# Kernel optimization log

Measured on AMD Instinct MI355X. Metric: run time of the kernel, lower is better.

Reference implementation:

```python
import jax, jax.numpy as jnp
import numpy as np

T = 32400   # bs*H*W BEV queries (1*180*180)
S = 16896   # bs*num_cams*h*w image keys (1*6*32*88)
E = 256     # embed_dim
H = 8       # num_heads
D = 32      # head_dim
MAXL = 32   # max interval length (ref_num_f)


def _mlp(x, w1, b1, w2, b2):
    # nn.Sequential(Linear(E,2E), ReLU, Linear(2E,E))
    return jax.nn.relu(x @ w1 + b1) @ w2 + b2


def setup_inputs() -> dict:
    k0 = jax.random.key(0)
    ks = jax.random.split(k0, 8)
    # ragged interval structure: every BEV cell has an interval of length (idx%32)+1
    lengths = (np.arange(T) % MAXL) + 1
    starts = np.concatenate([np.zeros(1, np.int64), np.cumsum(lengths)[:-1]])
    N = int(lengths.sum())  # 534472 frustum points
    ranks_bev = np.repeat(np.arange(T), lengths)          # sorted by BEV cell
    rng = np.random.default_rng(0)
    ranks_feat = rng.integers(0, S, size=N)               # which key/value row each point reads

    def lin(k, fi, fo):
        return jax.random.normal(k, (fi, fo), jnp.float32) * (1.0 / np.sqrt(fi))

    key_feat = jax.random.normal(ks[1], (S, E), jnp.float32)
    return dict(
        query_depth=jax.random.normal(ks[0], (T, E), jnp.float32),
        key=key_feat,
        value=key_feat,  # module asserts torch.equal(key, value)
        q_w1=lin(ks[2], E, 2 * E), q_b1=jnp.zeros((2 * E,), jnp.float32),
        q_w2=lin(ks[3], 2 * E, E), q_b2=jnp.zeros((E,), jnp.float32),
        k_w1=lin(ks[4], E, 2 * E), k_b1=jnp.zeros((2 * E,), jnp.float32),
        k_w2=lin(ks[5], 2 * E, E), k_b2=jnp.zeros((E,), jnp.float32),
        ranks_feat_f=jnp.asarray(ranks_feat, jnp.int32),
        ranks_bev_f=jnp.asarray(ranks_bev, jnp.int32),
        interval_starts_f=jnp.asarray(starts, jnp.int32),
        interval_lengths_f=jnp.asarray(lengths, jnp.int32),
        ref_num=MAXL,
    )


def reference(query_depth, key, value,
              q_w1, q_b1, q_w2, q_b2,
              k_w1, k_b1, k_w2, k_b2,
              ranks_feat_f, ranks_bev_f,
              interval_starts_f, interval_lengths_f, ref_num):
    scaling = 1.0 / jnp.sqrt(jnp.float32(D))
    q = (_mlp(query_depth, q_w1, q_b1, q_w2, q_b2) * scaling).reshape(T, H, D)
    k = _mlp(key, k_w1, k_b1, k_w2, k_b2).reshape(S, H, D)
    v = value.reshape(S, H, D)

    N = ranks_bev_f.shape[0]
    pt = jnp.arange(N, dtype=jnp.int32)
    # interval id of each point (intervals are contiguous, sorted by start)
    iid = jnp.searchsorted(interval_starts_f, pt, side='right') - 1
    ranks_ref = pt - interval_starts_f[iid]  # within-interval slot, in [0, ref_num)

    # per-point raw attention logit: q[bev] . k[feat] per head  -> [N, H]
    w = jnp.einsum('nhd,nhd->nh', q[ranks_bev_f], k[ranks_feat_f])

    # scatter into ragged weight tensor [T, H, ref_num]; padding masked to -1e9
    attn = jnp.full((T, H, ref_num), -1e9, jnp.float32)
    attn = attn.at[ranks_bev_f, :, ranks_ref].set(w)
    attn = jax.nn.softmax(attn, axis=-1)

    # gather normalized weights back per point and scatter-combine values
    wp = attn[ranks_bev_f, :, ranks_ref]          # [N, H]
    vp = v[ranks_feat_f]                          # [N, H, D]
    out = jnp.zeros((T, H, D), jnp.float32).at[ranks_bev_f].add(wp[:, :, None] * vp)
    return out.reshape(T, E)
```

## Files before the change

### kernel.cpp

```cpp
#include <hip/hip_runtime.h>
#include <hip/hip_bf16.h>
#include <cstdint>
#include <cstddef>

constexpr int T_Q   = 32400;
constexpr int T_PAD = 32512;
constexpr int S_K   = 16896;
constexpr int E_DIM = 256;
constexpr int HID   = 512;

typedef __bf16 bf16x8 __attribute__((ext_vector_type(8)));
typedef float  f32x4  __attribute__((ext_vector_type(4)));
typedef unsigned short ushort8v __attribute__((ext_vector_type(8)));

__device__ __forceinline__ void async16(const __hip_bfloat16* gp, __hip_bfloat16* lp) {
    __builtin_amdgcn_global_load_lds(
        (const __attribute__((address_space(1))) void*)(gp),
        (__attribute__((address_space(3))) void*)(lp), 16, 0, 0);
}

__device__ __forceinline__ float b2f(unsigned short u) {
    return __uint_as_float(((unsigned)u) << 16);
}

constexpr int NB_K = (S_K * E_DIM / 4) / 256;
constexpr int NB_PREP = NB_K + 128;

__global__ __launch_bounds__(256) void prep(
    const float* __restrict__ val_in,
    const float* __restrict__ s0, const float* __restrict__ s1,
    const float* __restrict__ s2, const float* __restrict__ s3,
    __hip_bfloat16* __restrict__ kvB,
    __hip_bfloat16* __restrict__ d0, __hip_bfloat16* __restrict__ d1,
    __hip_bfloat16* __restrict__ d2, __hip_bfloat16* __restrict__ d3) {
    __shared__ float tb[64][65];
    const int b = blockIdx.x;
    const int tid = threadIdx.x;

    if (b < NB_K) {
        int i = (b * 256 + tid) * 4;
        float4 f = *(const float4*)(val_in + i);
        union { ushort4 u4; __hip_bfloat16 bb[4]; } cv;
        cv.bb[0] = __float2bfloat16(f.x);
        cv.bb[1] = __float2bfloat16(f.y);
        cv.bb[2] = __float2bfloat16(f.z);
        cv.bb[3] = __float2bfloat16(f.w);
        int r = i >> 8, c = i & 255;
        *(ushort4*)(kvB + (size_t)r * 512 + 256 + c) = cv.u4;
        return;
    }

    int tloc = b - NB_K;
    int m = tloc >> 5;
    int tt = tloc & 31;
    const float* S = m == 0 ? s0 : m == 1 ? s1 : m == 2 ? s2 : s3;
    __hip_bfloat16* D = m == 0 ? d0 : m == 1 ? d1 : m == 2 ? d2 : d3;
    int Kd, Nd, kt, nt;
    if ((m & 1) == 0) { Kd = 256; Nd = 512; kt = tt & 3; nt = tt >> 2; }
    else              { Kd = 512; Nd = 256; kt = tt & 7; nt = tt >> 3; }
    int tx = tid & 63, ty = tid >> 6;
#pragma unroll
    for (int p = 0; p < 16; ++p) {
        int row = ty * 16 + p;
        tb[row][tx] = S[(size_t)(kt * 64 + row) * Nd + nt * 64 + tx];
    }
    __syncthreads();
#pragma unroll
    for (int p = 0; p < 16; ++p) {
        int row = ty * 16 + p;
        D[(size_t)(nt * 64 + row) * Kd + kt * 64 + tx] = __float2bfloat16(tb[tx][row]);
    }
}


constexpr int MLP_QT = T_PAD / 64;
constexpr int MLP_KT = S_K / 64;
constexpr int MLP_NB = MLP_QT + MLP_KT;

__global__ __launch_bounds__(512) void mlp_fused(
    const float* __restrict__ Aq, const float* __restrict__ Ak,
    const __hip_bfloat16* __restrict__ W1q, const __hip_bfloat16* __restrict__ W1k,
    const __hip_bfloat16* __restrict__ W2q, const __hip_bfloat16* __restrict__ W2k,
    const float* __restrict__ b1q, const float* __restrict__ b1k,
    const float* __restrict__ b2q, const float* __restrict__ b2k,
    __hip_bfloat16* __restrict__ Cq, __hip_bfloat16* __restrict__ Ck,
    float scaleq, int qtiles) {
    __shared__ __align__(16) __hip_bfloat16 As[64 * 256];
    __shared__ __align__(16) __hip_bfloat16 Hs[64 * 256];
    __shared__ __align__(16) __hip_bfloat16 Bsbuf[2][256 * 64];

    const int b = blockIdx.x;
    const bool isq = b < qtiles;
    const float* A  = isq ? Aq : Ak;
    const __hip_bfloat16* W1 = isq ? W1q : W1k;
    const __hip_bfloat16* W2 = isq ? W2q : W2k;
    const float* b1 = isq ? b1q : b1k;
    const float* b2 = isq ? b2q : b2k;
    __hip_bfloat16* C = isq ? Cq : Ck;
    const int ldc = isq ? E_DIM : 512;
    const float scale = isq ? scaleq : 1.0f;
    const int mrow0 = (isq ? b : b - qtiles) * 64;
    const int rowlim = isq ? T_Q : S_K;

    const int tid = threadIdx.x;
    const int w = tid >> 6, l = tid & 63;
    const int lm = l & 15, lq = l >> 4;
    const int wm = w >> 2;
    const int wn4 = w & 3;
    const int srow8 = l >> 3;
    const int u8 = l & 7;
    const int scolB = (u8 ^ srow8) << 3;

    auto issueW1 = [&](int nh, int st, int bi) {
#pragma unroll
        for (int c = 0; c < 4; ++c) {
            int r = w * 32 + c * 8 + srow8;
            async16(W1 + (size_t)(nh * 256 + r) * 256 + st * 64 + scolB,
                    Bsbuf[bi] + (w * 32 + c * 8) * 64);
        }
    };
    auto issueW2 = [&](int nh, int st, int bi) {
#pragma unroll
        for (int c = 0; c < 4; ++c) {
            int r = w * 32 + c * 8 + srow8;
            async16(W2 + (size_t)r * 512 + nh * 256 + st * 64 + scolB,
                    Bsbuf[bi] + (w * 32 + c * 8) * 64);
        }
    };

    issueW1(0, 0, 0);
#pragma unroll
    for (int c = 0; c < 4; ++c) {
        int idx = tid + c * 512;
        int row = idx >> 5;
        int u = idx & 31;
        int gr = mrow0 + row;
        float4 f0 = make_float4(0.f, 0.f, 0.f, 0.f);
        float4 f1 = make_float4(0.f, 0.f, 0.f, 0.f);
        if (gr < rowlim) {
            const float* ap = A + (size_t)gr * 256 + u * 8;
            f0 = *(const float4*)ap;
            f1 = *(const float4*)(ap + 4);
        }
        union { bf16x8 v; __hip_bfloat16 bb[8]; } cv;
        cv.bb[0] = __float2bfloat16(f0.x); cv.bb[1] = __float2bfloat16(f0.y);
        cv.bb[2] = __float2bfloat16(f0.z); cv.bb[3] = __float2bfloat16(f0.w);
        cv.bb[4] = __float2bfloat16(f1.x); cv.bb[5] = __float2bfloat16(f1.y);
        cv.bb[6] = __float2bfloat16(f1.z); cv.bb[7] = __float2bfloat16(f1.w);
        int pu = (u & 24) | ((u & 7) ^ (row & 7));
        *(bf16x8*)(As + row * 256 + pu * 8) = cv.v;
    }
    __syncthreads();

    int cur = 0;
    f32x4 acc2[2][4] = {};

#pragma unroll 1
    for (int nh = 0; nh < 2; ++nh) {
        f32x4 acc[2][4] = {};
#pragma unroll 1
        for (int st = 0; st < 4; ++st) {
            if (st < 3) issueW1(nh, st + 1, cur ^ 1);
            else        issueW2(nh, 0, cur ^ 1);
            const __hip_bfloat16* Bb = Bsbuf[cur];
#pragma unroll
            for (int ks = 0; ks < 2; ++ks) {
                bf16x8 af[2], bfr[4];
#pragma unroll
                for (int mi = 0; mi < 2; ++mi) {
                    int row = wm * 32 + mi * 16 + lm;
                    int un = st * 8 + ks * 4 + lq;
                    int pu = (un & 24) | ((un & 7) ^ (row & 7));
                    af[mi] = *(const bf16x8*)(As + row * 256 + pu * 8);
                }
#pragma unroll
                for (int ni = 0; ni < 4; ++ni) {
                    int brow = wn4 * 64 + ni * 16 + lm;
                    int pu = (ks * 4 + lq) ^ (brow & 7);
                    bfr[ni] = *(const bf16x8*)(Bb + brow * 64 + pu * 8);
                }
#pragma unroll
                for (int mi = 0; mi < 2; ++mi)
#pragma unroll
                    for (int ni = 0; ni < 4; ++ni)
                        acc[mi][ni] = __builtin_amdgcn_mfma_f32_16x16x32_bf16(
                            af[mi], bfr[ni], acc[mi][ni], 0, 0, 0);
            }
            __syncthreads();
            cur ^= 1;
        }

#pragma unroll
        for (int ni = 0; ni < 4; ++ni) {
            int col = wn4 * 64 + ni * 16 + lm;
            float bv = b1[nh * 256 + col];
            int un = col >> 3, el = col & 7;
#pragma unroll
            for (int mi = 0; mi < 2; ++mi) {
#pragma unroll
                for (int r = 0; r < 4; ++r) {
                    int row = wm * 32 + mi * 16 + lq * 4 + r;
                    float vv = fmaxf(acc[mi][ni][r] + bv, 0.f);
                    int pu = (un & 24) | ((un & 7) ^ (row & 7));
                    Hs[row * 256 + pu * 8 + el] = __float2bfloat16(vv);
                }
            }
        }
        __syncthreads();

#pragma unroll 1
        for (int st = 0; st < 4; ++st) {
            if (st < 3)          issueW2(nh, st + 1, cur ^ 1);
            else if (nh == 0)    issueW1(1, 0, cur ^ 1);
            const __hip_bfloat16* Bb = Bsbuf[cur];
#pragma unroll
            for (int ks = 0; ks < 2; ++ks) {
                bf16x8 af[2], bfr[4];
#pragma unroll
                for (int mi = 0; mi < 2; ++mi) {
                    int row = wm * 32 + mi * 16 + lm;
                    int un = st * 8 + ks * 4 + lq;
                    int pu = (un & 24) | ((un & 7) ^ (row & 7));
                    af[mi] = *(const bf16x8*)(Hs + row * 256 + pu * 8);
                }
#pragma unroll
                for (int ni = 0; ni < 4; ++ni) {
                    int brow = wn4 * 64 + ni * 16 + lm;
                    int pu = (ks * 4 + lq) ^ (brow & 7);
                    bfr[ni] = *(const bf16x8*)(Bb + brow * 64 + pu * 8);
                }
#pragma unroll
                for (int mi = 0; mi < 2; ++mi)
#pragma unroll
                    for (int ni = 0; ni < 4; ++ni)
                        acc2[mi][ni] = __builtin_amdgcn_mfma_f32_16x16x32_bf16(
                            af[mi], bfr[ni], acc2[mi][ni], 0, 0, 0);
            }
            __syncthreads();
            cur ^= 1;
        }
    }

#pragma unroll
    for (int ni = 0; ni < 4; ++ni) {
        int col = wn4 * 64 + ni * 16 + lm;
        float bv = b2[col];
#pragma unroll
        for (int mi = 0; mi < 2; ++mi) {
            size_t rowb = (size_t)mrow0 + wm * 32 + mi * 16 + lq * 4;
#pragma unroll
            for (int r = 0; r < 4; ++r) {
                float vv = (acc2[mi][ni][r] + bv) * scale;
                C[(rowb + r) * ldc + col] = __float2bfloat16(vv);
            }
        }
    }
}


#define PREFP(KB, VB, C)                                                     \
    {                                                                        \
        int f_ = __shfl(myf, (C) + half);                                    \
        const __hip_bfloat16* p_ = kv + ((size_t)f_ << 9) + (sub << 3);      \
        KB = *(const ushort8v*)p_;                                           \
        VB = *(const ushort8v*)(p_ + 256);                                   \
    }

#define PROCP(KB, VB, C)                                                     \
    {                                                                        \
        float wv = 0.f;                                                      \
        _Pragma("unroll") for (int i = 0; i < 8; ++i)                        \
            wv = fmaf(qf[i], b2f(KB[i]), wv);                                \
        wv += __shfl_xor(wv, 1);                                             \
        wv += __shfl_xor(wv, 2);                                             \
        float sc = ((C) + half < L) ? wv : -1e30f;                           \
        float so = __shfl_xor(sc, 32);                                       \
        float pm = fmaxf(sc, so);                                            \
        if (__all(pm <= m)) {                                                \
            float p = __expf(sc - m);                                        \
            s += p;                                                          \
            _Pragma("unroll") for (int i = 0; i < 8; ++i)                    \
                a[i] = fmaf(p, b2f(VB[i]), a[i]);                            \
        } else {                                                             \
            float mn = fmaxf(m, pm);                                         \
            float al = __expf(m - mn);                                       \
            float p  = __expf(sc - mn);                                      \
            m = mn;                                                          \
            s = fmaf(s, al, p);                                              \
            _Pragma("unroll") for (int i = 0; i < 8; ++i)                    \
                a[i] = fmaf(p, b2f(VB[i]), a[i] * al);                       \
        }                                                                    \
    }

#define STEPP(KB, VB, J)                                                     \
    if (c + (J) < L) {                                                       \
        PROCP(KB, VB, c + (J));                                              \
        if (c + (J) + 8 < L) PREFP(KB, VB, c + (J) + 8);                     \
    }

constexpr int ATTN_BLOCKS = 2026;

__global__ __launch_bounds__(256) void attn_kernel(
    const __hip_bfloat16* __restrict__ q,
    const __hip_bfloat16* __restrict__ kv,
    const int* __restrict__ rf,
    const int* __restrict__ starts,
    const int* __restrict__ lens,
    float* __restrict__ out) {
    const int wid = threadIdx.x >> 6;
    const int l = threadIdx.x & 63;
    const int sub = l & 31, half = l >> 5;
    const int tstride = gridDim.x * 4;

    for (int t = blockIdx.x * 4 + wid; t < T_Q; t += tstride) {
        int su = __builtin_amdgcn_readfirstlane(starts[t]);
        int L  = __builtin_amdgcn_readfirstlane(lens[t]);

        int li = l < L - 1 ? l : L - 1;
        int myf = rf[su + li];

        ushort8v qu = *(const ushort8v*)(q + (size_t)t * 256 + sub * 8);
        float qf[8];
#pragma unroll
        for (int i = 0; i < 8; ++i) qf[i] = b2f(qu[i]);

        float m = -INFINITY, s = 0.f;
        float a[8] = {0.f, 0.f, 0.f, 0.f, 0.f, 0.f, 0.f, 0.f};

        ushort8v k0 = {}, v0 = {}, k1 = {}, v1 = {};
        ushort8v k2 = {}, v2 = {}, k3 = {}, v3 = {};
        PREFP(k0, v0, 0);
        if (L > 2) PREFP(k1, v1, 2);
        if (L > 4) PREFP(k2, v2, 4);
        if (L > 6) PREFP(k3, v3, 6);

        for (int c = 0; c < L; c += 8) {
            STEPP(k0, v0, 0)
            STEPP(k1, v1, 2)
            STEPP(k2, v2, 4)
            STEPP(k3, v3, 6)
        }

        float st = s + __shfl_xor(s, 32);
#pragma unroll
        for (int i = 0; i < 8; ++i) a[i] += __shfl_xor(a[i], 32);

        if (half) {
            float inv = 1.f / st;
            float* op = out + (size_t)t * 256 + sub * 8;
            float4 o0, o1;
            o0.x = a[0] * inv; o0.y = a[1] * inv; o0.z = a[2] * inv; o0.w = a[3] * inv;
            o1.x = a[4] * inv; o1.y = a[5] * inv; o1.z = a[6] * inv; o1.w = a[7] * inv;
            *(float4*)op = o0;
            *(float4*)(op + 4) = o1;
        }
    }
}

extern "C" void kernel_launch(void* const* d_in, const int* in_sizes, int n_in,
                              void* d_out, int out_size, void* d_ws, size_t ws_size,
                              hipStream_t stream) {
    const float* q_in   = (const float*)d_in[0];
    const float* key_in = (const float*)d_in[1];
    const float* val_in = (const float*)d_in[2];
    const float* q_w1   = (const float*)d_in[3];
    const float* q_b1   = (const float*)d_in[4];
    const float* q_w2   = (const float*)d_in[5];
    const float* q_b2   = (const float*)d_in[6];
    const float* k_w1   = (const float*)d_in[7];
    const float* k_b1   = (const float*)d_in[8];
    const float* k_w2   = (const float*)d_in[9];
    const float* k_b2   = (const float*)d_in[10];
    const int* ranks_feat = (const int*)d_in[11];
    const int* starts     = (const int*)d_in[13];
    const int* lens       = (const int*)d_in[14];
    float* out = (float*)d_out;

    char* ws = (char*)d_ws;
    size_t off = 0;
    auto alloc = [&](size_t bytes) {
        char* p = ws + off;
        off += (bytes + 255) & ~(size_t)255;
        return p;
    };
    __hip_bfloat16* qMl  = (__hip_bfloat16*)alloc((size_t)T_PAD * E_DIM * 2);
    __hip_bfloat16* kvB  = (__hip_bfloat16*)alloc((size_t)S_K * 512 * 2);
    __hip_bfloat16* w1qT = (__hip_bfloat16*)alloc((size_t)HID * E_DIM * 2);
    __hip_bfloat16* w2qT = (__hip_bfloat16*)alloc((size_t)E_DIM * HID * 2);
    __hip_bfloat16* w1kT = (__hip_bfloat16*)alloc((size_t)HID * E_DIM * 2);
    __hip_bfloat16* w2kT = (__hip_bfloat16*)alloc((size_t)E_DIM * HID * 2);
    (void)ws_size; (void)n_in; (void)out_size; (void)in_sizes;

    prep<<<NB_PREP, 256, 0, stream>>>(val_in, q_w1, q_w2, k_w1, k_w2,
                                      kvB, w1qT, w2qT, w1kT, w2kT);

    const float qscale = 0.17677669529663687f;

    mlp_fused<<<MLP_NB, 512, 0, stream>>>(
        q_in, key_in, w1qT, w1kT, w2qT, w2kT,
        q_b1, k_b1, q_b2, k_b2, qMl, kvB, qscale, MLP_QT);

    attn_kernel<<<ATTN_BLOCKS, 256, 0, stream>>>(qMl, kvB, ranks_feat, starts, lens, out);
}
```

Before: 270.6 us.

## Replace double-buffered weight staging with single larger K-chunk load per stage

The fused MLP kernel previously staged W1/W2 in two 64-wide K-chunk LDS buffers and prefetched the next chunk while computing the current one. It now loads one 128-wide K-chunk into a single buffer, waits on a barrier, computes, then syncs. This halves the number of stage iterations and barriers, but it drops the overlap between global-to-LDS weight loads and MFMA compute, so load latency is exposed in every stage.

```diff
diff --git a/kernel.cpp b/kernel.cpp
--- a/kernel.cpp
+++ b/kernel.cpp
@@ -87,7 +87,7 @@
     float scaleq, int qtiles) {
     __shared__ __align__(16) __hip_bfloat16 As[64 * 256];
     __shared__ __align__(16) __hip_bfloat16 Hs[64 * 256];
-    __shared__ __align__(16) __hip_bfloat16 Bsbuf[2][256 * 64];
+    __shared__ __align__(16) __hip_bfloat16 Bs[256 * 128];
 
     const int b = blockIdx.x;
     const bool isq = b < qtiles;
@@ -107,28 +107,9 @@
     const int lm = l & 15, lq = l >> 4;
     const int wm = w >> 2;
     const int wn4 = w & 3;
-    const int srow8 = l >> 3;
-    const int u8 = l & 7;
-    const int scolB = (u8 ^ srow8) << 3;
-
-    auto issueW1 = [&](int nh, int st, int bi) {
-#pragma unroll
-        for (int c = 0; c < 4; ++c) {
-            int r = w * 32 + c * 8 + srow8;
-            async16(W1 + (size_t)(nh * 256 + r) * 256 + st * 64 + scolB,
-                    Bsbuf[bi] + (w * 32 + c * 8) * 64);
-        }
-    };
-    auto issueW2 = [&](int nh, int st, int bi) {
-#pragma unroll
-        for (int c = 0; c < 4; ++c) {
-            int r = w * 32 + c * 8 + srow8;
-            async16(W2 + (size_t)r * 512 + nh * 256 + st * 64 + scolB,
-                    Bsbuf[bi] + (w * 32 + c * 8) * 64);
-        }
-    };
-
-    issueW1(0, 0, 0);
+    const int r4 = l >> 4;
+    const int sl = l & 15;
+
 #pragma unroll
     for (int c = 0; c < 4; ++c) {
         int idx = tid + c * 512;
@@ -152,32 +133,38 @@
     }
     __syncthreads();
 
-    int cur = 0;
     f32x4 acc2[2][4] = {};
 
 #pragma unroll 1
     for (int nh = 0; nh < 2; ++nh) {
         f32x4 acc[2][4] = {};
 #pragma unroll 1
-        for (int st = 0; st < 4; ++st) {
-            if (st < 3) issueW1(nh, st + 1, cur ^ 1);
-            else        issueW2(nh, 0, cur ^ 1);
-            const __hip_bfloat16* Bb = Bsbuf[cur];
-#pragma unroll
-            for (int ks = 0; ks < 2; ++ks) {
+        for (int st = 0; st < 2; ++st) {
+#pragma unroll
+            for (int c = 0; c < 8; ++c) {
+                int rbase = w * 32 + c * 4;
+                int row = rbase + r4;
+                int gcol = (((sl & 8) | ((sl & 7) ^ (row & 7)))) << 3;
+                async16(W1 + (size_t)(nh * 256 + row) * 256 + st * 128 + gcol,
+                        Bs + rbase * 128);
+            }
+            __syncthreads();
+#pragma unroll
+            for (int ks = 0; ks < 4; ++ks) {
                 bf16x8 af[2], bfr[4];
 #pragma unroll
                 for (int mi = 0; mi < 2; ++mi) {
                     int row = wm * 32 + mi * 16 + lm;
-                    int un = st * 8 + ks * 4 + lq;
+                    int un = st * 16 + ks * 4 + lq;
                     int pu = (un & 24) | ((un & 7) ^ (row & 7));
                     af[mi] = *(const bf16x8*)(As + row * 256 + pu * 8);
                 }
 #pragma unroll
                 for (int ni = 0; ni < 4; ++ni) {
                     int brow = wn4 * 64 + ni * 16 + lm;
-                    int pu = (ks * 4 + lq) ^ (brow & 7);
-                    bfr[ni] = *(const bf16x8*)(Bb + brow * 64 + pu * 8);
+                    int un = ks * 4 + lq;
+                    int pu = (un & 8) | ((un & 7) ^ (brow & 7));
+                    bfr[ni] = *(const bf16x8*)(Bs + brow * 128 + pu * 8);
                 }
 #pragma unroll
                 for (int mi = 0; mi < 2; ++mi)
@@ -187,7 +174,6 @@
                             af[mi], bfr[ni], acc[mi][ni], 0, 0, 0);
             }
             __syncthreads();
-            cur ^= 1;
         }
 
 #pragma unroll
@@ -209,25 +195,32 @@
         __syncthreads();
 
 #pragma unroll 1
-        for (int st = 0; st < 4; ++st) {
-            if (st < 3)          issueW2(nh, st + 1, cur ^ 1);
-            else if (nh == 0)    issueW1(1, 0, cur ^ 1);
-            const __hip_bfloat16* Bb = Bsbuf[cur];
-#pragma unroll
-            for (int ks = 0; ks < 2; ++ks) {
+        for (int st = 0; st < 2; ++st) {
+#pragma unroll
+            for (int c = 0; c < 8; ++c) {
+                int rbase = w * 32 + c * 4;
+                int row = rbase + r4;
+                int gcol = (((sl & 8) | ((sl & 7) ^ (row & 7)))) << 3;
+                async16(W2 + (size_t)row * 512 + nh * 256 + st * 128 + gcol,
+                        Bs + rbase * 128);
+            }
+            __syncthreads();
+#pragma unroll
+            for (int ks = 0; ks < 4; ++ks) {
                 bf16x8 af[2], bfr[4];
 #pragma unroll
                 for (int mi = 0; mi < 2; ++mi) {
                     int row = wm * 32 + mi * 16 + lm;
-                    int un = st * 8 + ks * 4 + lq;
+                    int un = st * 16 + ks * 4 + lq;
                     int pu = (un & 24) | ((un & 7) ^ (row & 7));
                     af[mi] = *(const bf16x8*)(Hs + row * 256 + pu * 8);
                 }
 #pragma unroll
                 for (int ni = 0; ni < 4; ++ni) {
                     int brow = wn4 * 64 + ni * 16 + lm;
-                    int pu = (ks * 4 + lq) ^ (brow & 7);
-                    bfr[ni] = *(const bf16x8*)(Bb + brow * 64 + pu * 8);
+                    int un = ks * 4 + lq;
+                    int pu = (un & 8) | ((un & 7) ^ (brow & 7));
+                    bfr[ni] = *(const bf16x8*)(Bs + brow * 128 + pu * 8);
                 }
 #pragma unroll
                 for (int mi = 0; mi < 2; ++mi)
@@ -237,7 +230,6 @@
                             af[mi], bfr[ni], acc2[mi][ni], 0, 0, 0);
             }
             __syncthreads();
-            cur ^= 1;
         }
     }
 
```

New measurement: 274.8 us. No clear change (+1.6%).
